# Kernel tuning notes

Hardware: AMD Instinct MI355X
Metric: run time of the kernel (lower is better)

The kernel has to match this reference:

```python
import jax, jax.numpy as jnp
import numpy as np

B, L, D_IN, D_MODEL, D_STATE, D_DISCR, KER = 2, 1024, 512, 1024, 16, 64, 4


def setup_inputs() -> dict:
    ks = jax.random.split(jax.random.key(0), 9)
    s = 0.02
    return {
        "seq": jax.random.normal(ks[0], (B, L, D_IN), jnp.float32),
        "W_in": jax.random.normal(ks[1], (2 * D_MODEL, D_IN), jnp.float32) * s,
        "W_out": jax.random.normal(ks[2], (D_IN, D_MODEL), jnp.float32) * s,
        "W_B": jax.random.normal(ks[3], (D_STATE, D_MODEL), jnp.float32) * s,
        "W_C": jax.random.normal(ks[4], (D_STATE, D_MODEL), jnp.float32) * s,
        "W_D1": jax.random.normal(ks[5], (D_DISCR, D_MODEL), jnp.float32) * s,
        "W_D2": jax.random.normal(ks[6], (D_MODEL, D_DISCR), jnp.float32) * s,
        "conv_w": jax.random.normal(ks[7], (D_MODEL, 1, KER), jnp.float32) * 0.1,
        "conv_b": jax.random.normal(ks[8], (D_MODEL,), jnp.float32) * 0.01,
        "A": jnp.tile(jnp.arange(1, D_STATE + 1, dtype=jnp.float32), (D_MODEL, 1)),
        "D": jnp.ones((D_MODEL,), jnp.float32),
    }


def _causal_depthwise_conv(x, w, b):
    # x: [B, L, D] -> torch Conv1d(groups=D, padding=KER-1) truncated to first L outputs
    x = jnp.swapaxes(x, 1, 2)  # [B, D, L]
    y = jax.lax.conv_general_dilated(
        x, w, window_strides=(1,), padding=[(KER - 1, 0)],
        dimension_numbers=("NCH", "OIH", "NCH"), feature_group_count=D_MODEL)
    y = y + b[None, :, None]
    return jnp.swapaxes(y, 1, 2)  # [B, L, D]


def _ssm(x, W_B, W_C, W_D1, W_D2, A, D):
    # x: [B, L, D]
    exp_negA = jnp.exp(-A)                                  # [D, S]
    Bm = jnp.einsum("bld,sd->bls", x, W_B)                  # [B, L, S]
    Cm = jnp.einsum("bld,sd->bls", x, W_C)                  # [B, L, S]
    delta = jax.nn.softplus(D + jnp.einsum("ble,de->bld", jnp.einsum("bld,ed->ble", x, W_D1), W_D2))  # [B, L, D]
    A_bar = exp_negA[None, None] * delta[..., None]         # [B, L, D, S]
    X = Bm[:, :, None, :] * delta[..., None] * x[..., None]  # [B, L, D, S]

    def comb(c1, c2):
        a1, x1 = c1
        a2, x2 = c2
        return a1 * a2, a2 * x1 + x2

    _, h = jax.lax.associative_scan(comb, (A_bar, X), axis=1)  # h: [B, L, D, S]
    y = jnp.einsum("blds,bls->bld", h, Cm)
    return y + D * x


def reference(seq, W_in, W_out, W_B, W_C, W_D1, W_D2, conv_w, conv_b, A, D):
    ab = jnp.einsum("bli,oi->blo", seq, W_in)   # [B, L, 2*D_MODEL]
    a, b = ab[..., :D_MODEL], ab[..., D_MODEL:]
    a = jax.nn.silu(_causal_depthwise_conv(a, conv_w, conv_b))
    a = _ssm(a, W_B, W_C, W_D1, W_D2, A, D)
    out = a * jax.nn.silu(b)
    return jnp.einsum("bld,od->blo", out, W_out)  # [B, L, D_IN]
```

## Files before the change

### kernel.cpp

```cpp
#include <hip/hip_runtime.h>
#include <hip/hip_bf16.h>

typedef short short8 __attribute__((ext_vector_type(8)));
typedef float float4v __attribute__((ext_vector_type(4)));

#define B_   2
#define L_   1024
#define DIN  512
#define DM   1024
#define DS   16
#define DD   64
#define KER_ 4
#define NROW (B_*L_)

#define SD   4
#define SC   64
#define SLC  16
#define SDP  5

__device__ __forceinline__ float silu_f(float v){ return v / (1.f + expf(-v)); }

__device__ __forceinline__ short2 f2bf2(float a, float b) {
  __hip_bfloat162 h = __float22bfloat162_rn(float2{a, b});
  union { __hip_bfloat162 h; short2 s; } u; u.h = h; return u.s;
}
__device__ __forceinline__ short8 pack8(const float4& x0, const float4& x1) {
  short2 s0 = f2bf2(x0.x, x0.y), s1 = f2bf2(x0.z, x0.w);
  short2 s2 = f2bf2(x1.x, x1.y), s3 = f2bf2(x1.z, x1.w);
  return short8{ s0.x, s0.y, s1.x, s1.y, s2.x, s2.y, s3.x, s3.y };
}
__device__ __forceinline__ float bf2f(short s) {
  union { unsigned u; float f; } v; v.u = ((unsigned)(unsigned short)s) << 16; return v.f;
}

__global__ __launch_bounds__(256)
void gemm1_k(const float* __restrict__ seq, const float* __restrict__ Win,
             __hip_bfloat16* __restrict__ ab) {
  __shared__ short As[64 * 40];
  __shared__ short Bs[64 * 40];
  const int tid  = threadIdx.x;
  const int lane = tid & 63;
  const int wave = tid >> 6;
  const int r16  = lane & 15;
  const int quad = lane >> 4;
  const int m0 = blockIdx.y * 64;
  const int n0 = blockIdx.x * 64;
  const int wm = wave & 1, wn = wave >> 1;
  float4v acc[2][2];
#pragma unroll
  for (int i = 0; i < 2; i++)
#pragma unroll
    for (int j = 0; j < 2; j++) acc[i][j] = (float4v){0.f, 0.f, 0.f, 0.f};
  float4 pf0[2], pf1[2];
  auto ldu = [&](int j, int k0) {
    int u = tid + j * 256;
    const float4* p;
    if (u < 256) { int row = u >> 2, q = u & 3;
      p = (const float4*)(seq + (size_t)(m0 + row) * DIN + k0 + q * 8);
    } else { int v = u - 256; int row = v >> 2, q = v & 3;
      p = (const float4*)(Win + (size_t)(n0 + row) * DIN + k0 + q * 8);
    }
    pf0[j] = p[0]; pf1[j] = p[1];
  };
  auto stu = [&](int j) {
    int u = tid + j * 256;
    short8 s = pack8(pf0[j], pf1[j]);
    if (u < 256) { int row = u >> 2, q = u & 3; *(short8*)&As[row * 40 + q * 8] = s; }
    else { int v = u - 256; int row = v >> 2, q = v & 3; *(short8*)&Bs[row * 40 + q * 8] = s; }
  };
  ldu(0, 0); ldu(1, 0);
  for (int k0 = 0; k0 < DIN; k0 += 32) {
    stu(0); stu(1);
    __syncthreads();
    if (k0 + 32 < DIN) { ldu(0, k0 + 32); ldu(1, k0 + 32); }
    short8 afr[2], bfr[2];
#pragma unroll
    for (int mi = 0; mi < 2; mi++)
      afr[mi] = *(const short8*)&As[(wm * 32 + mi * 16 + r16) * 40 + quad * 8];
#pragma unroll
    for (int ni = 0; ni < 2; ni++)
      bfr[ni] = *(const short8*)&Bs[(wn * 32 + ni * 16 + r16) * 40 + quad * 8];
#pragma unroll
    for (int mi = 0; mi < 2; mi++)
#pragma unroll
      for (int ni = 0; ni < 2; ni++)
        acc[mi][ni] = __builtin_amdgcn_mfma_f32_16x16x32_bf16(afr[mi], bfr[ni], acc[mi][ni], 0, 0, 0);
    __syncthreads();
  }
#pragma unroll
  for (int mi = 0; mi < 2; mi++)
#pragma unroll
    for (int ni = 0; ni < 2; ni++) {
      int gn = n0 + wn * 32 + ni * 16 + r16;
#pragma unroll
      for (int r = 0; r < 4; r++) {
        int gm = m0 + wm * 32 + mi * 16 + quad * 4 + r;
        ab[(size_t)gm * (2 * DM) + gn] = __float2bfloat16(acc[mi][ni][r]);
      }
    }
}

__global__ __launch_bounds__(256)
void proj_k(const __hip_bfloat16* __restrict__ ab, const float* __restrict__ WB,
            const float* __restrict__ WC, const float* __restrict__ WD1,
            const float* __restrict__ cw, const float* __restrict__ cb,
            float* __restrict__ pall) {
  __shared__ short As[64 * 40];
  __shared__ short Bs[96 * 40];
  const int tid  = threadIdx.x;
  const int lane = tid & 63;
  const int wave = tid >> 6;
  const int r16  = lane & 15;
  const int quad = lane >> 4;
  const int m0   = blockIdx.y * 64;
  const int kbeg = blockIdx.z * 128;
  float4v acc[6];
#pragma unroll
  for (int i = 0; i < 6; i++) acc[i] = (float4v){0.f, 0.f, 0.f, 0.f};

  short8 ta[KER_];
  float4 pf0[2], pf1[2];

  const int arow = tid >> 2, aq = tid & 3;
  const int an = m0 + arow, al = an & (L_ - 1), abq = an >> 10;

  auto ldu_a = [&](int k0) {
#pragma unroll
    for (int t = 0; t < KER_; t++) {
      int ll = al - (KER_ - 1) + t;
      if (ll >= 0)
        ta[t] = *(const short8*)(ab + (size_t)(abq * L_ + ll) * (2 * DM) + k0 + aq * 8);
      else
        ta[t] = short8{0,0,0,0,0,0,0,0};
    }
  };
  auto stu_a = [&](int k0) {
    float r8[8];
#pragma unroll
    for (int e = 0; e < 8; e++) {
      int d = k0 + aq * 8 + e;
      float4 w = *(const float4*)(cw + d * 4);
      float a = cb[d];
      a += bf2f(ta[0][e]) * w.x;
      a += bf2f(ta[1][e]) * w.y;
      a += bf2f(ta[2][e]) * w.z;
      a += bf2f(ta[3][e]) * w.w;
      r8[e] = silu_f(a);
    }
    *(short8*)&As[arow * 40 + aq * 8] =
        pack8(float4{r8[0], r8[1], r8[2], r8[3]}, float4{r8[4], r8[5], r8[6], r8[7]});
  };
  auto ldu_b = [&](int j, int k0) {
    int u = tid + j * 256;
    if (u >= 640) return;
    int v = u - 256, row = v >> 2, q = v & 3;
    const float* bp = (row < 16) ? (WB + (size_t)row * DM)
                    : (row < 32) ? (WC + (size_t)(row - 16) * DM)
                                 : (WD1 + (size_t)(row - 32) * DM);
    const float4* p = (const float4*)(bp + k0 + q * 8);
    pf0[j - 1] = p[0]; pf1[j - 1] = p[1];
  };
  auto stu_b = [&](int j) {
    int u = tid + j * 256;
    if (u >= 640) return;
    int v = u - 256, row = v >> 2, q = v & 3;
    *(short8*)&Bs[row * 40 + q * 8] = pack8(pf0[j - 1], pf1[j - 1]);
  };

  ldu_a(kbeg); ldu_b(1, kbeg); ldu_b(2, kbeg);
  for (int k0 = kbeg; k0 < kbeg + 128; k0 += 32) {
    stu_a(k0); stu_b(1); stu_b(2);
    __syncthreads();
    if (k0 + 32 < kbeg + 128) { ldu_a(k0 + 32); ldu_b(1, k0 + 32); ldu_b(2, k0 + 32); }
    short8 afr = *(const short8*)&As[(wave * 16 + r16) * 40 + quad * 8];
#pragma unroll
    for (int ni = 0; ni < 6; ni++) {
      short8 bfr = *(const short8*)&Bs[(ni * 16 + r16) * 40 + quad * 8];
      acc[ni] = __builtin_amdgcn_mfma_f32_16x16x32_bf16(afr, bfr, acc[ni], 0, 0, 0);
    }
    __syncthreads();
  }
#pragma unroll
  for (int ni = 0; ni < 6; ni++) {
    int gn = ni * 16 + r16;
#pragma unroll
    for (int r = 0; r < 4; r++) {
      int gm = m0 + wave * 16 + quad * 4 + r;
      atomicAdd(&pall[(size_t)gm * 96 + gn], acc[ni][r]);
    }
  }
}

__global__ __launch_bounds__(256)
void delta_k(const float* __restrict__ t1, const float* __restrict__ WD2,
             const float* __restrict__ Dv, float* __restrict__ dlt) {
  __shared__ short As[64 * 40];
  __shared__ short Bs[64 * 40];
  const int tid  = threadIdx.x;
  const int lane = tid & 63;
  const int wave = tid >> 6;
  const int r16  = lane & 15;
  const int quad = lane >> 4;
  const int m0 = blockIdx.y * 64;
  const int n0 = blockIdx.x * 64;
  const int wm = wave & 1, wn = wave >> 1;
  float4v acc[2][2];
#pragma unroll
  for (int i = 0; i < 2; i++)
#pragma unroll
    for (int j = 0; j < 2; j++) acc[i][j] = (float4v){0.f, 0.f, 0.f, 0.f};
  float4 pf0[2], pf1[2];
  auto ldu = [&](int j, int k0) {
    int u = tid + j * 256;
    const float4* p;
    if (u < 256) { int row = u >> 2, q = u & 3;
      p = (const float4*)(t1 + (size_t)(m0 + row) * 96 + k0 + q * 8);
    } else { int v = u - 256; int row = v >> 2, q = v & 3;
      p = (const float4*)(WD2 + (size_t)(n0 + row) * DD + k0 + q * 8);
    }
    pf0[j] = p[0]; pf1[j] = p[1];
  };
  auto stu = [&](int j) {
    int u = tid + j * 256;
    short8 s = pack8(pf0[j], pf1[j]);
    if (u < 256) { int row = u >> 2, q = u & 3; *(short8*)&As[row * 40 + q * 8] = s; }
    else { int v = u - 256; int row = v >> 2, q = v & 3; *(short8*)&Bs[row * 40 + q * 8] = s; }
  };
  ldu(0, 0); ldu(1, 0);
  for (int k0 = 0; k0 < DD; k0 += 32) {
    stu(0); stu(1);
    __syncthreads();
    if (k0 + 32 < DD) { ldu(0, k0 + 32); ldu(1, k0 + 32); }
    short8 afr[2], bfr[2];
#pragma unroll
    for (int mi = 0; mi < 2; mi++)
      afr[mi] = *(const short8*)&As[(wm * 32 + mi * 16 + r16) * 40 + quad * 8];
#pragma unroll
    for (int ni = 0; ni < 2; ni++)
      bfr[ni] = *(const short8*)&Bs[(wn * 32 + ni * 16 + r16) * 40 + quad * 8];
#pragma unroll
    for (int mi = 0; mi < 2; mi++)
#pragma unroll
      for (int ni = 0; ni < 2; ni++)
        acc[mi][ni] = __builtin_amdgcn_mfma_f32_16x16x32_bf16(afr[mi], bfr[ni], acc[mi][ni], 0, 0, 0);
    __syncthreads();
  }
#pragma unroll
  for (int mi = 0; mi < 2; mi++)
#pragma unroll
    for (int ni = 0; ni < 2; ni++) {
      int gn = n0 + wn * 32 + ni * 16 + r16;
      float dvn = Dv[gn];
#pragma unroll
      for (int r = 0; r < 4; r++) {
        int gm = m0 + wm * 32 + mi * 16 + quad * 4 + r;
        float v = acc[mi][ni][r] + dvn;
        v = fmaxf(v, 0.f) + log1pf(expf(-fabsf(v)));
        dlt[(size_t)gm * DM + gn] = v;
      }
    }
}

__global__ __launch_bounds__(256)
void scan_fused_k(const __hip_bfloat16* __restrict__ ab, const float* __restrict__ dlt,
                  const float* __restrict__ pall, const float* __restrict__ A,
                  const float* __restrict__ Dv, const float* __restrict__ cw,
                  const float* __restrict__ cb, float* __restrict__ sout) {
  __shared__ float Pl[SC][DS][SDP];
  __shared__ float Hl[SC][DS][SDP];
  const int blk = blockIdx.x;
  const int b   = blk >> 8;
  const int d0  = (blk & 255) * SD;
  const int dd  = threadIdx.x & (SD - 1);
  const int c   = threadIdx.x >> 2;
  const int d   = d0 + dd;

  float e[DS];
#pragma unroll
  for (int s = 0; s < DS; s++) e[s] = expf(-A[d * DS + s]);
  const int   lbase = c * SLC;
  const int   nbase = b * L_ + lbase;
  const float4 w    = *(const float4*)(cw + d * 4);
  const float  cbv  = cb[d];

  auto abA = [&](int l) -> float {
    return (l >= 0) ? __bfloat162float(ab[(size_t)(b * L_ + l) * (2 * DM) + d]) : 0.f;
  };

  float r0 = abA(lbase - 3), r1 = abA(lbase - 2), r2 = abA(lbase - 1);
  float h[DS], p[DS];
#pragma unroll
  for (int s = 0; s < DS; s++) { h[s] = 0.f; p[s] = 1.f; }
  for (int i = 0; i < SLC; i++) {
    int n = nbase + i;
    float a3 = __bfloat162float(ab[(size_t)n * (2 * DM) + d]);
    float xv = silu_f(cbv + r0 * w.x + r1 * w.y + r2 * w.z + a3 * w.w);
    r0 = r1; r1 = r2; r2 = a3;
    float dl = dlt[(size_t)n * DM + d];
    float dx = dl * xv;
    const float4* bm4 = (const float4*)(pall + (size_t)n * 96);
    float4 b0 = bm4[0], b1 = bm4[1], b2 = bm4[2], b3 = bm4[3];
    float bmv[DS] = { b0.x,b0.y,b0.z,b0.w, b1.x,b1.y,b1.z,b1.w,
                      b2.x,b2.y,b2.z,b2.w, b3.x,b3.y,b3.z,b3.w };
#pragma unroll
    for (int s = 0; s < DS; s++) {
      float a_ = e[s] * dl;
      h[s] = a_ * h[s] + bmv[s] * dx;
      p[s] *= a_;
    }
  }
#pragma unroll
  for (int s = 0; s < DS; s++) { Pl[c][s][dd] = p[s]; Hl[c][s][dd] = h[s]; }
  __syncthreads();

  if (threadIdx.x < DS * SD) {
    int s2  = threadIdx.x >> 2;
    int dd2 = threadIdx.x & (SD - 1);
    float H = 0.f;
    for (int c2 = 0; c2 < SC; c2++) {
      float pp = Pl[c2][s2][dd2];
      float hh = Hl[c2][s2][dd2];
      Pl[c2][s2][dd2] = H;
      H = pp * H + hh;
    }
  }
  __syncthreads();

#pragma unroll
  for (int s = 0; s < DS; s++) h[s] = Pl[c][s][dd];
  float Dd = Dv[d];
  r0 = abA(lbase - 3); r1 = abA(lbase - 2); r2 = abA(lbase - 1);
  for (int i = 0; i < SLC; i++) {
    int n = nbase + i;
    float a3 = __bfloat162float(ab[(size_t)n * (2 * DM) + d]);
    float xv = silu_f(cbv + r0 * w.x + r1 * w.y + r2 * w.z + a3 * w.w);
    r0 = r1; r1 = r2; r2 = a3;
    float dl = dlt[(size_t)n * DM + d];
    float dx = dl * xv;
    const float4* bm4 = (const float4*)(pall + (size_t)n * 96);
    float4 b0 = bm4[0], b1 = bm4[1], b2 = bm4[2], b3 = bm4[3];
    float4 c0 = bm4[4], c1 = bm4[5], c2v = bm4[6], c3 = bm4[7];
    float bmv[DS] = { b0.x,b0.y,b0.z,b0.w, b1.x,b1.y,b1.z,b1.w,
                      b2.x,b2.y,b2.z,b2.w, b3.x,b3.y,b3.z,b3.w };
    float cmv[DS] = { c0.x,c0.y,c0.z,c0.w, c1.x,c1.y,c1.z,c1.w,
                      c2v.x,c2v.y,c2v.z,c2v.w, c3.x,c3.y,c3.z,c3.w };
    float y = 0.f;
#pragma unroll
    for (int s = 0; s < DS; s++) {
      h[s] = e[s] * dl * h[s] + bmv[s] * dx;
      y += h[s] * cmv[s];
    }
    y += Dd * xv;
    float g = __bfloat162float(ab[(size_t)n * (2 * DM) + DM + d]);
    sout[(size_t)n * DM + d] = y * silu_f(g);
  }
}

__global__ __launch_bounds__(512)
void gemm2_k(const float* __restrict__ sout, const float* __restrict__ Wout,
             float* __restrict__ out) {
  __shared__ short As[64 * 40];
  __shared__ short Bs[64 * 40];
  const int tid  = threadIdx.x;
  const int lane = tid & 63;
  const int wave = tid >> 6;
  const int r16  = lane & 15;
  const int quad = lane >> 4;
  const int m0 = blockIdx.y * 64;
  const int n0 = blockIdx.x * 64;
  const int wm = wave & 1, wn = wave >> 1;
  float4v acc[2];
  acc[0] = (float4v){0.f, 0.f, 0.f, 0.f};
  acc[1] = (float4v){0.f, 0.f, 0.f, 0.f};
  float4 pf0, pf1;
  auto ldu = [&](int k0) {
    const float4* p;
    if (tid < 256) { int row = tid >> 2, q = tid & 3;
      p = (const float4*)(sout + (size_t)(m0 + row) * DM + k0 + q * 8);
    } else { int v = tid - 256; int row = v >> 2, q = v & 3;
      p = (const float4*)(Wout + (size_t)(n0 + row) * DM + k0 + q * 8);
    }
    pf0 = p[0]; pf1 = p[1];
  };
  auto stu = [&]() {
    short8 s = pack8(pf0, pf1);
    if (tid < 256) { int row = tid >> 2, q = tid & 3; *(short8*)&As[row * 40 + q * 8] = s; }
    else { int v = tid - 256; int row = v >> 2, q = v & 3; *(short8*)&Bs[row * 40 + q * 8] = s; }
  };
  ldu(0);
  for (int k0 = 0; k0 < DM; k0 += 32) {
    stu();
    __syncthreads();
    if (k0 + 32 < DM) ldu(k0 + 32);
    short8 afr[2], bfr;
    afr[0] = *(const short8*)&As[(wm * 32 + r16) * 40 + quad * 8];
    afr[1] = *(const short8*)&As[(wm * 32 + 16 + r16) * 40 + quad * 8];
    bfr    = *(const short8*)&Bs[(wn * 16 + r16) * 40 + quad * 8];
    acc[0] = __builtin_amdgcn_mfma_f32_16x16x32_bf16(afr[0], bfr, acc[0], 0, 0, 0);
    acc[1] = __builtin_amdgcn_mfma_f32_16x16x32_bf16(afr[1], bfr, acc[1], 0, 0, 0);
    __syncthreads();
  }
#pragma unroll
  for (int mi = 0; mi < 2; mi++)
#pragma unroll
    for (int r = 0; r < 4; r++)
      out[(size_t)(m0 + wm * 32 + mi * 16 + quad * 4 + r) * DIN + n0 + wn * 16 + r16] = acc[mi][r];
}

extern "C" void kernel_launch(void* const* d_in, const int* in_sizes, int n_in,
                              void* d_out, int out_size, void* d_ws, size_t ws_size,
                              hipStream_t stream) {
  const float* seq  = (const float*)d_in[0];
  const float* Win  = (const float*)d_in[1];
  const float* Wout = (const float*)d_in[2];
  const float* WB   = (const float*)d_in[3];
  const float* WC   = (const float*)d_in[4];
  const float* WD1  = (const float*)d_in[5];
  const float* WD2  = (const float*)d_in[6];
  const float* cw   = (const float*)d_in[7];
  const float* cb   = (const float*)d_in[8];
  const float* A    = (const float*)d_in[9];
  const float* Dv   = (const float*)d_in[10];
  float* out = (float*)d_out;

  float* ws = (float*)d_ws;
  __hip_bfloat16* ab = (__hip_bfloat16*)ws;
  float* dlt  = ws   + 2097152;
  float* pall = dlt  + 2097152;
  float* sout = pall + 196608;
  float* t1   = pall + 32;

  hipMemsetAsync(pall, 0, (size_t)NROW * 96 * 4, stream);
  gemm1_k<<<dim3(32, 32), 256, 0, stream>>>(seq, Win, ab);
  proj_k<<<dim3(1, 32, 8), 256, 0, stream>>>(ab, WB, WC, WD1, cw, cb, pall);
  delta_k<<<dim3(16, 32), 256, 0, stream>>>(t1, WD2, Dv, dlt);
  scan_fused_k<<<B_ * (DM / SD), 256, 0, stream>>>(ab, dlt, pall, A, Dv, cw, cb, sout);
  gemm2_k<<<dim3(8, 32), 512, 0, stream>>>(sout, Wout, out);
}
```

Before: 179.9 us.

## Precompute conv+silu and gate into transposed buffers for the scan

Adds a kernel that computes the causal depthwise conv with silu and copies the gate half, both written transposed as [d][n]. delta_k also now writes delta transposed. The scan kernel reads these per-channel rows instead of recomputing the conv, and its blocking changes to 8 channels × 32 chunks of 32 steps. This removes the redundant conv recompute done in both scan passes, at the cost of an extra kernel, extra workspace traffic and strided stores in delta_k.

```diff
diff --git a/kernel.cpp b/kernel.cpp
--- a/kernel.cpp
+++ b/kernel.cpp
@@ -13,10 +13,10 @@
 #define KER_ 4
 #define NROW (B_*L_)
 
-#define SD   4
-#define SC   64
-#define SLC  16
-#define SDP  5
+#define SD   8
+#define SC   32
+#define SLC  32
+#define SDP  9
 
 __device__ __forceinline__ float silu_f(float v){ return v / (1.f + expf(-v)); }
 
@@ -98,6 +98,47 @@
         ab[(size_t)gm * (2 * DM) + gn] = __float2bfloat16(acc[mi][ni][r]);
       }
     }
+}
+
+__global__ __launch_bounds__(256)
+void convT_k(const __hip_bfloat16* __restrict__ ab, const float* __restrict__ cw,
+             const float* __restrict__ cb, float* __restrict__ xt,
+             short* __restrict__ gt) {
+  __shared__ short tile[67 * 74];
+  const int n0 = blockIdx.x * 64;
+  const int d0 = blockIdx.y * 64;
+  const int l0 = n0 & (L_ - 1);
+  for (int u = threadIdx.x; u < 67 * 8; u += 256) {
+    int r = u >> 3, c8 = u & 7;
+    int l = l0 - 3 + r;
+    short8 v = short8{0, 0, 0, 0, 0, 0, 0, 0};
+    if (l >= 0 && r < 67)
+      v = *(const short8*)(ab + (size_t)(n0 - l0 + l) * (2 * DM) + d0 + c8 * 8);
+    *(short8*)&tile[r * 74 + c8 * 8] = v;
+  }
+  __syncthreads();
+  const int i  = threadIdx.x & 63;
+  const int dl = threadIdx.x >> 6;
+  if (d0 < DM) {
+#pragma unroll 4
+    for (int p = 0; p < 16; p++) {
+      int dc = p * 4 + dl;
+      int d  = d0 + dc;
+      float4 w = *(const float4*)(cw + d * 4);
+      float a = cb[d];
+      a += bf2f(tile[(i + 0) * 74 + dc]) * w.x;
+      a += bf2f(tile[(i + 1) * 74 + dc]) * w.y;
+      a += bf2f(tile[(i + 2) * 74 + dc]) * w.z;
+      a += bf2f(tile[(i + 3) * 74 + dc]) * w.w;
+      xt[(size_t)d * NROW + n0 + i] = silu_f(a);
+    }
+  } else {
+#pragma unroll 4
+    for (int p = 0; p < 16; p++) {
+      int dc = p * 4 + dl;
+      gt[(size_t)(d0 - DM + dc) * NROW + n0 + i] = tile[(i + 3) * 74 + dc];
+    }
+  }
 }
 
 __global__ __launch_bounds__(256)
@@ -120,7 +161,6 @@
 
   short8 ta[KER_];
   float4 pf0[2], pf1[2];
-
   const int arow = tid >> 2, aq = tid & 3;
   const int an = m0 + arow, al = an & (L_ - 1), abq = an >> 10;
 
@@ -131,7 +171,7 @@
       if (ll >= 0)
         ta[t] = *(const short8*)(ab + (size_t)(abq * L_ + ll) * (2 * DM) + k0 + aq * 8);
       else
-        ta[t] = short8{0,0,0,0,0,0,0,0};
+        ta[t] = short8{0, 0, 0, 0, 0, 0, 0, 0};
     }
   };
   auto stu_a = [&](int k0) {
@@ -193,7 +233,7 @@
 
 __global__ __launch_bounds__(256)
 void delta_k(const float* __restrict__ t1, const float* __restrict__ WD2,
-             const float* __restrict__ Dv, float* __restrict__ dlt) {
+             const float* __restrict__ Dv, float* __restrict__ dltT) {
   __shared__ short As[64 * 40];
   __shared__ short Bs[64 * 40];
   const int tid  = threadIdx.x;
@@ -256,47 +296,40 @@
         int gm = m0 + wm * 32 + mi * 16 + quad * 4 + r;
         float v = acc[mi][ni][r] + dvn;
         v = fmaxf(v, 0.f) + log1pf(expf(-fabsf(v)));
-        dlt[(size_t)gm * DM + gn] = v;
+        dltT[(size_t)gn * NROW + gm] = v;
       }
     }
 }
 
 __global__ __launch_bounds__(256)
-void scan_fused_k(const __hip_bfloat16* __restrict__ ab, const float* __restrict__ dlt,
+void scan_fused_k(const float* __restrict__ xt, const float* __restrict__ dltT,
                   const float* __restrict__ pall, const float* __restrict__ A,
-                  const float* __restrict__ Dv, const float* __restrict__ cw,
-                  const float* __restrict__ cb, float* __restrict__ sout) {
+                  const float* __restrict__ Dv, const short* __restrict__ gt,
+                  float* __restrict__ sout) {
   __shared__ float Pl[SC][DS][SDP];
   __shared__ float Hl[SC][DS][SDP];
   const int blk = blockIdx.x;
-  const int b   = blk >> 8;
-  const int d0  = (blk & 255) * SD;
+  const int b   = blk >> 7;
+  const int d0  = (blk & 127) * SD;
   const int dd  = threadIdx.x & (SD - 1);
-  const int c   = threadIdx.x >> 2;
+  const int c   = threadIdx.x >> 3;
   const int d   = d0 + dd;
 
   float e[DS];
 #pragma unroll
   for (int s = 0; s < DS; s++) e[s] = expf(-A[d * DS + s]);
-  const int   lbase = c * SLC;
-  const int   nbase = b * L_ + lbase;
-  const float4 w    = *(const float4*)(cw + d * 4);
-  const float  cbv  = cb[d];
-
-  auto abA = [&](int l) -> float {
-    return (l >= 0) ? __bfloat162float(ab[(size_t)(b * L_ + l) * (2 * DM) + d]) : 0.f;
-  };
-
-  float r0 = abA(lbase - 3), r1 = abA(lbase - 2), r2 = abA(lbase - 1);
+  const int nbase = b * L_ + c * SLC;
+  const float* xrow = xt   + (size_t)d * NROW;
+  const float* drow = dltT + (size_t)d * NROW;
+  const short* grow = gt   + (size_t)d * NROW;
+
   float h[DS], p[DS];
 #pragma unroll
   for (int s = 0; s < DS; s++) { h[s] = 0.f; p[s] = 1.f; }
   for (int i = 0; i < SLC; i++) {
     int n = nbase + i;
-    float a3 = __bfloat162float(ab[(size_t)n * (2 * DM) + d]);
-    float xv = silu_f(cbv + r0 * w.x + r1 * w.y + r2 * w.z + a3 * w.w);
-    r0 = r1; r1 = r2; r2 = a3;
-    float dl = dlt[(size_t)n * DM + d];
+    float dl = drow[n];
+    float xv = xrow[n];
     float dx = dl * xv;
     const float4* bm4 = (const float4*)(pall + (size_t)n * 96);
     float4 b0 = bm4[0], b1 = bm4[1], b2 = bm4[2], b3 = bm4[3];
@@ -314,7 +347,7 @@
   __syncthreads();
 
   if (threadIdx.x < DS * SD) {
-    int s2  = threadIdx.x >> 2;
+    int s2  = threadIdx.x >> 3;
     int dd2 = threadIdx.x & (SD - 1);
     float H = 0.f;
     for (int c2 = 0; c2 < SC; c2++) {
@@ -329,13 +362,10 @@
 #pragma unroll
   for (int s = 0; s < DS; s++) h[s] = Pl[c][s][dd];
   float Dd = Dv[d];
-  r0 = abA(lbase - 3); r1 = abA(lbase - 2); r2 = abA(lbase - 1);
   for (int i = 0; i < SLC; i++) {
     int n = nbase + i;
-    float a3 = __bfloat162float(ab[(size_t)n * (2 * DM) + d]);
-    float xv = silu_f(cbv + r0 * w.x + r1 * w.y + r2 * w.z + a3 * w.w);
-    r0 = r1; r1 = r2; r2 = a3;
-    float dl = dlt[(size_t)n * DM + d];
+    float dl = drow[n];
+    float xv = xrow[n];
     float dx = dl * xv;
     const float4* bm4 = (const float4*)(pall + (size_t)n * 96);
     float4 b0 = bm4[0], b1 = bm4[1], b2 = bm4[2], b3 = bm4[3];
@@ -351,7 +381,7 @@
       y += h[s] * cmv[s];
     }
     y += Dd * xv;
-    float g = __bfloat162float(ab[(size_t)n * (2 * DM) + DM + d]);
+    float g = bf2f(grow[n]);
     sout[(size_t)n * DM + d] = y * silu_f(g);
   }
 }
@@ -425,15 +455,18 @@
 
   float* ws = (float*)d_ws;
   __hip_bfloat16* ab = (__hip_bfloat16*)ws;
-  float* dlt  = ws   + 2097152;
-  float* pall = dlt  + 2097152;
+  float* xt   = ws   + 2097152;
+  short* gt   = (short*)(xt + 2097152);
+  float* dltT = (float*)(gt + 2097152);
+  float* pall = dltT + 2097152;
   float* sout = pall + 196608;
   float* t1   = pall + 32;
 
   hipMemsetAsync(pall, 0, (size_t)NROW * 96 * 4, stream);
   gemm1_k<<<dim3(32, 32), 256, 0, stream>>>(seq, Win, ab);
+  convT_k<<<dim3(NROW / 64, (2 * DM) / 64), 256, 0, stream>>>(ab, cw, cb, xt, gt);
   proj_k<<<dim3(1, 32, 8), 256, 0, stream>>>(ab, WB, WC, WD1, cw, cb, pall);
-  delta_k<<<dim3(16, 32), 256, 0, stream>>>(t1, WD2, Dv, dlt);
-  scan_fused_k<<<B_ * (DM / SD), 256, 0, stream>>>(ab, dlt, pall, A, Dv, cw, cb, sout);
+  delta_k<<<dim3(16, 32), 256, 0, stream>>>(t1, WD2, Dv, dltT);
+  scan_fused_k<<<B_ * (DM / SD), 256, 0, stream>>>(xt, dltT, pall, A, Dv, gt, sout);
   gemm2_k<<<dim3(8, 32), 512, 0, stream>>>(sout, Wout, out);
 }
```

Measured after the change: 191.0 us. +6.2%, slower.
